# Kernel optimization log

Hardware: AMD Instinct MI355X
Metric: run time of the kernel (lower is better)

The kernel has to match this reference:

```python
import math
import jax, jax.numpy as jnp
import numpy as np

B, C, H, W = 8, 512, 32, 32
HEADS = 8


def _mix_rot(re, im, Wm, phi):
    # nn.Linear(dim, dim, bias=False) applied channelwise on [B,C,H,W]:
    # y = x @ Wm.T  ->  einsum over input channel c, output channel d
    re2 = jnp.einsum('bchw,dc->bdhw', re, Wm)
    im2 = jnp.einsum('bchw,dc->bdhw', im, Wm)
    c = jnp.cos(phi)[None, :, None, None]
    s = jnp.sin(phi)[None, :, None, None]
    # complex multiply (re2 + i*im2) * (cos phi + i*sin phi)
    return re2 * c - im2 * s, re2 * s + im2 * c


def setup_inputs() -> dict:
    key = jax.random.key(0)
    ks = jax.random.split(key, 6)
    scale = 1.0 / math.sqrt(C)
    return {
        'z_re': jax.random.normal(ks[0], (B, C, H, W), jnp.float32),
        'z_im': jax.random.normal(ks[1], (B, C, H, W), jnp.float32),
        'Wq': jax.random.normal(ks[2], (C, C), jnp.float32) * scale,
        'phi_q': jnp.zeros((C,), jnp.float32),
        'Wk': jax.random.normal(ks[3], (C, C), jnp.float32) * scale,
        'phi_k': jnp.zeros((C,), jnp.float32),
        'Wv': jax.random.normal(ks[4], (C, C), jnp.float32) * scale,
        'phi_v': jnp.zeros((C,), jnp.float32),
        'Wo': jax.random.normal(ks[5], (C, C), jnp.float32) * scale,
        'phi_o': jnp.zeros((C,), jnp.float32),
    }


def reference(z_re, z_im, Wq, phi_q, Wk, phi_k, Wv, phi_v, Wo, phi_o):
    b, c, h, w = z_re.shape
    T = h * w
    dh = c // HEADS

    def tok(a):  # [B,C,H,W] -> [B,T,C]
        return a.reshape(b, c, T).transpose(0, 2, 1)

    qre, qim = _mix_rot(z_re, z_im, Wq, phi_q)
    kre, kim = _mix_rot(z_re, z_im, Wk, phi_k)
    vre, vim = _mix_rot(z_re, z_im, Wv, phi_v)
    qre, qim = tok(qre), tok(qim)
    kre, kim = tok(kre), tok(kim)
    vre, vim = tok(vre), tok(vim)

    # real part of complex inner product: sums over FULL channel dim (no head split)
    scores = (jnp.einsum('btc,buc->btu', qre, kre)
              + jnp.einsum('btc,buc->btu', qim, kim)) / math.sqrt(dh)
    causal = jnp.triu(jnp.ones((T, T), bool), k=1)
    scores = jnp.where(causal[None], -jnp.inf, scores)
    attn = jax.nn.softmax(scores, axis=-1)

    out_re = jnp.einsum('btu,buc->btc', attn, vre)
    out_im = jnp.einsum('btu,buc->btc', attn, vim)

    def grid(a):  # [B,T,C] -> [B,C,H,W]
        return a.transpose(0, 2, 1).reshape(b, c, h, w)

    return _mix_rot(grid(out_re), grid(out_im), Wo, phi_o)
```

## Files before the change

kernel.cpp:

```cpp
#include <hip/hip_runtime.h>
#include <math.h>

#define NB 8
#define NC 512
#define NT 1024
#define BT (NB * NT)
#define SCALE 0.125f
#define NEG_BIG (-3.0e38f)

typedef __attribute__((ext_vector_type(8))) short short8v;
typedef __attribute__((ext_vector_type(8))) _Float16 half8v;
typedef __attribute__((ext_vector_type(4))) float float4v;
#define MFMA_BF16(A, B, C) __builtin_amdgcn_mfma_f32_16x16x32_bf16(A, B, C, 0, 0, 0)
#define MFMA_F16(A, B, C)  __builtin_amdgcn_mfma_f32_16x16x32_f16(A, B, C, 0, 0, 0)

__device__ __forceinline__ ushort f2bf(float f) {
    union { float f; unsigned int i; } v; v.f = f;
    unsigned int r = v.i + 0x7FFFu + ((v.i >> 16) & 1u);
    return (ushort)(r >> 16);
}

__device__ __forceinline__ ushort f2h(float f) {
    return __builtin_bit_cast(unsigned short, (_Float16)f);
}

__device__ __forceinline__ half8v scale8(short8v raw, float s) {
    half8v h = __builtin_bit_cast(half8v, raw);
    const _Float16 hs = (_Float16)s;
    half8v r;
    #pragma unroll
    for (int q = 0; q < 8; ++q) r[q] = h[q] * hs;
    return r;
}

#if defined(__has_builtin)
#if __has_builtin(__builtin_amdgcn_global_load_lds)
#define HAS_GLDS 1
#endif
#endif

#ifdef HAS_GLDS
__device__ __forceinline__ void glds16(const ushort* g, ushort* l) {
    __builtin_amdgcn_global_load_lds(
        (const __attribute__((address_space(1))) unsigned int*)g,
        (__attribute__((address_space(3))) unsigned int*)l, 16, 0, 0);
}
#endif

template<int ROWS>
__device__ __forceinline__ void stage64(const ushort* __restrict__ g, int rsShorts,
                                        ushort* tile, int w, int lane) {
    const int r8 = lane >> 3;
    const int ck = (lane & 7) ^ r8;
    const ushort* gl = g + (size_t)r8 * rsShorts + (ck << 3);
    constexpr int ni = ROWS / 32;
    #pragma unroll
    for (int s = 0; s < ni; ++s) {
        const int issue = w * ni + s;
#ifdef HAS_GLDS
        glds16(gl + (size_t)issue * 8 * rsShorts, tile + issue * 512);
#else
        const uint4 v = *(const uint4*)(gl + (size_t)issue * 8 * rsShorts);
        *(uint4*)(tile + issue * 512 + lane * 8) = v;
#endif
    }
}

__device__ __forceinline__ short8v frag(const ushort* tile, int rr, int q) {
    return *(const short8v*)(tile + rr * 64 + ((q ^ (rr & 7)) << 3));
}

__global__ __launch_bounds__(256) void prep_z_kernel(
    const float* __restrict__ zre, const float* __restrict__ zim,
    ushort* __restrict__ Z)
{
    const int t0 = blockIdx.x << 6, c0 = blockIdx.y << 6;
    const int bz = blockIdx.z, b = bz & 7, comp = bz >> 3;
    const float* src = (comp ? zim : zre) + (size_t)b * NC * NT;
    ushort* dst = Z + (size_t)(comp * NB + b) * NT * NC;
    const int tid = threadIdx.x;

    __shared__ ushort T[64][72];
    #pragma unroll
    for (int r = 0; r < 4; ++r) {
        const int cl = (tid >> 4) + r * 16;
        const int t4 = (tid & 15) << 2;
        const float4 v = *(const float4*)(src + (size_t)(c0 + cl) * NT + t0 + t4);
        T[t4 + 0][cl] = f2bf(v.x); T[t4 + 1][cl] = f2bf(v.y);
        T[t4 + 2][cl] = f2bf(v.z); T[t4 + 3][cl] = f2bf(v.w);
    }
    __syncthreads();
    const int tl = tid >> 2, cc = (tid & 3) << 4;
    ushort* op = dst + (size_t)(t0 + tl) * NC + c0 + cc;
    *(uint4*)op       = *(const uint4*)&T[tl][cc];
    *(uint4*)(op + 8) = *(const uint4*)&T[tl][cc + 8];
}

__global__ __launch_bounds__(256) void prep_w_kernel(
    const float* __restrict__ Wq, const float* __restrict__ Wk,
    const float* __restrict__ Wv, const float* __restrict__ Wo,
    ushort* __restrict__ Wbf)
{
    const int idx = blockIdx.x * 256 + threadIdx.x;
    const int e4 = idx << 2;
    const int m = e4 >> 18;
    const int off = e4 & ((1 << 18) - 1);
    const float* Ws[4] = {Wq, Wk, Wv, Wo};
    const float4 v = *(const float4*)(Ws[m] + off);
    ushort4 o;
    o.x = f2bf(v.x); o.y = f2bf(v.y); o.z = f2bf(v.z); o.w = f2bf(v.w);
    *(ushort4*)(Wbf + ((size_t)m << 18) + off) = o;
}

__global__ __launch_bounds__(256, 2) void proj_qk_kernel(
    const ushort* __restrict__ Z, const ushort* __restrict__ Wbf,
    const float* __restrict__ phiq, const float* __restrict__ phik,
    ushort* __restrict__ qre, ushort* __restrict__ qim,
    ushort* __restrict__ kre, ushort* __restrict__ kim)
{
    const int tid = threadIdx.x;
    const int m0 = blockIdx.x << 7;
    const int d0 = blockIdx.y << 6;
    const size_t NE = (size_t)BT * NC;

    __shared__ alignas(16) ushort SM[24576];
    ushort* Zr   = SM;
    ushort* Zi   = SM + 8192;
    ushort* Wq_s = SM + 16384;
    ushort* Wk_s = SM + 20480;
    uint*   R    = (uint*)SM;

    float4v accq[2][4][2] = {};
    float4v acck[2][4][2] = {};

    const int w = tid >> 6, lane = tid & 63;
    const int l15 = lane & 15, quad = lane >> 4;
    const int wm = (w & 1) << 6;
    const int wn = (w >> 1) << 5;

    for (int c0 = 0; c0 < NC; c0 += 64) {
        stage64<128>(Z + (size_t)m0 * NC + c0, NC, Zr, w, lane);
        stage64<128>(Z + NE + (size_t)m0 * NC + c0, NC, Zi, w, lane);
        stage64<64>(Wbf + (size_t)d0 * NC + c0, NC, Wq_s, w, lane);
        stage64<64>(Wbf + ((size_t)1 << 18) + (size_t)d0 * NC + c0, NC, Wk_s, w, lane);
        __syncthreads();
        #pragma unroll
        for (int kk = 0; kk < 2; ++kk) {
            const int q0 = kk * 4 + quad;
            short8v zf[2][4], wqf[2], wkf[2];
            #pragma unroll
            for (int i = 0; i < 4; ++i) {
                zf[0][i] = frag(Zr, wm + i * 16 + l15, q0);
                zf[1][i] = frag(Zi, wm + i * 16 + l15, q0);
            }
            #pragma unroll
            for (int j = 0; j < 2; ++j) {
                wqf[j] = frag(Wq_s, wn + j * 16 + l15, q0);
                wkf[j] = frag(Wk_s, wn + j * 16 + l15, q0);
            }
            #pragma unroll
            for (int c = 0; c < 2; ++c)
                #pragma unroll
                for (int i = 0; i < 4; ++i)
                    #pragma unroll
                    for (int j = 0; j < 2; ++j) {
                        accq[c][i][j] = MFMA_BF16(zf[c][i], wqf[j], accq[c][i][j]);
                        acck[c][i][j] = MFMA_BF16(zf[c][i], wkf[j], acck[c][i][j]);
                    }
        }
        __syncthreads();
    }

    float cq[2], sq[2], ck2[2], sk2[2];
    #pragma unroll
    for (int j = 0; j < 2; ++j) {
        const int d = d0 + wn + j * 16 + l15;
        const float pq = phiq[d], pk = phik[d];
        cq[j] = cosf(pq); sq[j] = sinf(pq);
        ck2[j] = cosf(pk); sk2[j] = sinf(pk);
    }
    const int g = tid >> 4, cl = tid & 15;

    #pragma unroll
    for (int j = 0; j < 2; ++j)
        #pragma unroll
        for (int i = 0; i < 4; ++i)
            #pragma unroll
            for (int r = 0; r < 4; ++r) {
                const int row = wm + i * 16 + quad * 4 + r;
                const int col = wn + j * 16 + l15;
                const float ar = accq[0][i][j][r], ai = accq[1][i][j][r];
                R[row * 76 + col] = (uint)f2bf(ar * cq[j] - ai * sq[j])
                                  | ((uint)f2bf(ar * sq[j] + ai * cq[j]) << 16);
            }
    __syncthreads();
    #pragma unroll
    for (int s = 0; s < 8; ++s) {
        const int row = g * 8 + s;
        const uint4 p = *(const uint4*)&R[row * 76 + cl * 4];
        uint2 re, im;
        re.x = (p.x & 0xFFFFu) | (p.y << 16);
        re.y = (p.z & 0xFFFFu) | (p.w << 16);
        im.x = (p.x >> 16) | (p.y & 0xFFFF0000u);
        im.y = (p.z >> 16) | (p.w & 0xFFFF0000u);
        const size_t off = (size_t)(m0 + row) * NC + d0 + cl * 4;
        *(uint2*)(qre + off) = re;
        *(uint2*)(qim + off) = im;
    }
    __syncthreads();

    #pragma unroll
    for (int j = 0; j < 2; ++j)
        #pragma unroll
        for (int i = 0; i < 4; ++i)
            #pragma unroll
            for (int r = 0; r < 4; ++r) {
                const int row = wm + i * 16 + quad * 4 + r;
                const int col = wn + j * 16 + l15;
                const float br = acck[0][i][j][r], bi = acck[1][i][j][r];
                R[row * 76 + col] = (uint)f2bf(br * ck2[j] - bi * sk2[j])
                                  | ((uint)f2bf(br * sk2[j] + bi * ck2[j]) << 16);
            }
    __syncthreads();
    #pragma unroll
    for (int s = 0; s < 8; ++s) {
        const int row = g * 8 + s;
        const uint4 p = *(const uint4*)&R[row * 76 + cl * 4];
        uint2 re, im;
        re.x = (p.x & 0xFFFFu) | (p.y << 16);
        re.y = (p.z & 0xFFFFu) | (p.w << 16);
        im.x = (p.x >> 16) | (p.y & 0xFFFF0000u);
        im.y = (p.z >> 16) | (p.w & 0xFFFF0000u);
        const size_t off = (size_t)(m0 + row) * NC + d0 + cl * 4;
        *(uint2*)(kre + off) = re;
        *(uint2*)(kim + off) = im;
    }
}

__global__ __launch_bounds__(256, 3) void proj_v_kernel(
    const ushort* __restrict__ Z, const ushort* __restrict__ Wbf,
    const float* __restrict__ phiv,
    ushort* __restrict__ vre, ushort* __restrict__ vim)
{
    const int tid = threadIdx.x;
    const int d0 = blockIdx.x << 7;
    const int bt0 = blockIdx.y << 6;
    const size_t NE = (size_t)BT * NC;

    __shared__ alignas(16) ushort SM[19456];
    ushort* Wv_s = SM;
    ushort* Zr   = SM + 8192;
    ushort* Zi   = SM + 12288;
    uint*   R    = (uint*)SM;

    float4v acc[2][4][2] = {};

    const int w = tid >> 6, lane = tid & 63;
    const int l15 = lane & 15, quad = lane >> 4;
    const int wm = (w & 1) << 6;
    const int wn = (w >> 1) << 5;

    for (int c0 = 0; c0 < NC; c0 += 64) {
        stage64<128>(Wbf + ((size_t)2 << 18) + (size_t)d0 * NC + c0, NC, Wv_s, w, lane);
        stage64<64>(Z + (size_t)bt0 * NC + c0, NC, Zr, w, lane);
        stage64<64>(Z + NE + (size_t)bt0 * NC + c0, NC, Zi, w, lane);
        __syncthreads();
        #pragma unroll
        for (int kk = 0; kk < 2; ++kk) {
            const int q0 = kk * 4 + quad;
            short8v wvf[4], zf[2][2];
            #pragma unroll
            for (int i = 0; i < 4; ++i)
                wvf[i] = frag(Wv_s, wm + i * 16 + l15, q0);
            #pragma unroll
            for (int j = 0; j < 2; ++j) {
                zf[0][j] = frag(Zr, wn + j * 16 + l15, q0);
                zf[1][j] = frag(Zi, wn + j * 16 + l15, q0);
            }
            #pragma unroll
            for (int c = 0; c < 2; ++c)
                #pragma unroll
                for (int i = 0; i < 4; ++i)
                    #pragma unroll
                    for (int j = 0; j < 2; ++j)
                        acc[c][i][j] = MFMA_BF16(wvf[i], zf[c][j], acc[c][i][j]);
        }
        __syncthreads();
    }

    const int d_own = d0 + wm + (l15 >> 2) * 16 + quad * 4 + (l15 & 3);
    const float ph_own = phiv[d_own];
    const float c_own = cosf(ph_own), s_own = sinf(ph_own);

    #pragma unroll
    for (int i = 0; i < 4; ++i)
        #pragma unroll
        for (int r = 0; r < 4; ++r) {
            const int src = (lane & 48) | (i * 4 + r);
            const float cs = __shfl(c_own, src, 64);
            const float sn = __shfl(s_own, src, 64);
            const int row = wm + i * 16 + quad * 4 + r;
            #pragma unroll
            for (int j = 0; j < 2; ++j) {
                const int col = wn + j * 16 + l15;
                const float vr = acc[0][i][j][r], vi = acc[1][i][j][r];
                R[row * 76 + col] = (uint)f2h(vr * cs - vi * sn)
                                  | ((uint)f2h(vr * sn + vi * cs) << 16);
            }
        }
    __syncthreads();
    const int g = tid >> 4, cl = tid & 15;
    const int b = bt0 >> 10, t0 = bt0 & 1023;
    #pragma unroll
    for (int s = 0; s < 8; ++s) {
        const int row = g * 8 + s;
        const uint4 p = *(const uint4*)&R[row * 76 + cl * 4];
        uint2 re, im;
        re.x = (p.x & 0xFFFFu) | (p.y << 16);
        re.y = (p.z & 0xFFFFu) | (p.w << 16);
        im.x = (p.x >> 16) | (p.y & 0xFFFF0000u);
        im.y = (p.z >> 16) | (p.w & 0xFFFF0000u);
        const size_t off = (size_t)b * NC * NT + (size_t)(d0 + row) * NT + t0 + cl * 4;
        *(uint2*)(vre + off) = re;
        *(uint2*)(vim + off) = im;
    }
}

__global__ __launch_bounds__(256, 3) void scores_kernel(
    const ushort* __restrict__ qre, const ushort* __restrict__ qim,
    const ushort* __restrict__ kre, const ushort* __restrict__ kim,
    ushort* __restrict__ Pp, float2* __restrict__ stats)
{
    const int u0b = blockIdx.x << 7;
    const int t0b = (gridDim.y - 1 - blockIdx.y) << 7;
    if (u0b > t0b) return;
    const int b = blockIdx.z;
    const int tid = threadIdx.x;
    const size_t qb = (size_t)b * NT * NC;

    __shared__ alignas(16) ushort SM[32768];
    ushort* Qr = SM;
    ushort* Qi = SM + 8192;
    ushort* Kr = SM + 16384;
    ushort* Ki = SM + 24576;
    ushort* Rs = SM;

    float4v acc[4][4] = {};

    const int w = tid >> 6, lane = tid & 63;
    const int l15 = lane & 15, quad = lane >> 4;
    const int wm = (w & 1) << 6;
    const int wn = (w >> 1) << 6;

    for (int c0 = 0; c0 < NC; c0 += 64) {
        stage64<128>(qre + qb + (size_t)t0b * NC + c0, NC, Qr, w, lane);
        stage64<128>(qim + qb + (size_t)t0b * NC + c0, NC, Qi, w, lane);
        stage64<128>(kre + qb + (size_t)u0b * NC + c0, NC, Kr, w, lane);
        stage64<128>(kim + qb + (size_t)u0b * NC + c0, NC, Ki, w, lane);
        __syncthreads();
        #pragma unroll
        for (int kk = 0; kk < 2; ++kk) {
            const int q0 = kk * 4 + quad;
            short8v qf[2][4], kf[2][4];
            #pragma unroll
            for (int i = 0; i < 4; ++i) {
                qf[0][i] = frag(Qr, wm + i * 16 + l15, q0);
                qf[1][i] = frag(Qi, wm + i * 16 + l15, q0);
                kf[0][i] = frag(Kr, wn + i * 16 + l15, q0);
                kf[1][i] = frag(Ki, wn + i * 16 + l15, q0);
            }
            #pragma unroll
            for (int i = 0; i < 4; ++i)
                #pragma unroll
                for (int j = 0; j < 4; ++j) {
                    acc[i][j] = MFMA_BF16(qf[0][i], kf[0][j], acc[i][j]);
                    acc[i][j] = MFMA_BF16(qf[1][i], kf[1][j], acc[i][j]);
                }
        }
        __syncthreads();
    }

    const int sub = (u0b + wn) >> 6;
    float2* st = stats + (size_t)(b * 16 + sub) * NT;
    #pragma unroll
    for (int i = 0; i < 4; ++i)
        #pragma unroll
        for (int r = 0; r < 4; ++r) {
            const int t = t0b + wm + i * 16 + quad * 4 + r;
            float v[4]; float m = NEG_BIG;
            #pragma unroll
            for (int j = 0; j < 4; ++j) {
                const int u = u0b + wn + j * 16 + l15;
                const float x = (u > t) ? NEG_BIG : acc[i][j][r] * SCALE;
                v[j] = x; m = fmaxf(m, x);
            }
            #pragma unroll
            for (int d = 1; d < 16; d <<= 1) m = fmaxf(m, __shfl_xor(m, d, 64));
            float l = 0.f;
            const int row = wm + i * 16 + quad * 4 + r;
            #pragma unroll
            for (int j = 0; j < 4; ++j) {
                const float e = __expf(v[j] - m);
                l += e;
                Rs[row * 140 + wn + j * 16 + l15] = f2h(e);
            }
            #pragma unroll
            for (int d = 1; d < 16; d <<= 1) l += __shfl_xor(l, d, 64);
            if (l15 == 0) st[t] = make_float2(m, l);
        }
    __syncthreads();
    ushort* Pb = Pp + (size_t)b * NT * NT;
    const int g = tid >> 5, cl = tid & 31;
    #pragma unroll
    for (int s = 0; s < 16; ++s) {
        const int row = g * 16 + s;
        const uint2 p = *(const uint2*)&Rs[row * 140 + cl * 4];
        *(uint2*)(Pb + (size_t)(t0b + row) * NT + u0b + cl * 4) = p;
    }
}

__global__ __launch_bounds__(256, 3) void pv_kernel(
    const ushort* __restrict__ Pp, const float2* __restrict__ stats,
    const ushort* __restrict__ vre, const ushort* __restrict__ vim,
    ushort* __restrict__ Ore, ushort* __restrict__ Oim)
{
    const int c0b = blockIdx.x << 6;
    const int t0b = (gridDim.y - 1 - blockIdx.y) << 7;
    const int b = blockIdx.z;
    const int tid = threadIdx.x;
    const ushort* P = Pp + ((size_t)b * NT + t0b) * NT;
    const size_t vb = (size_t)b * NC * NT;
    const int iters = (t0b + 128) >> 6;

    __shared__ alignas(16) ushort SM[20736];
    ushort* Ps = SM;
    ushort* Vr = SM + 8192;
    ushort* Vi = SM + 12288;
    float* sLds = (float*)(SM + 16384);
    uint*  R    = (uint*)SM;

    float4v acc[2][4][2] = {};

    const int w = tid >> 6, lane = tid & 63;
    const int l15 = lane & 15, quad = lane >> 4;
    const int wm = (w & 1) << 6;
    const int wn = (w >> 1) << 5;

    if (tid < 128) {
        const int t = t0b + tid;
        float mv[16], lv[16];
        #pragma unroll
        for (int s = 0; s < 16; ++s) {
            if (s < iters) {
                const float2 v = stats[(size_t)(b * 16 + s) * NT + t];
                mv[s] = v.x; lv[s] = v.y;
            } else { mv[s] = NEG_BIG; lv[s] = 0.f; }
        }
        float M = NEG_BIG;
        #pragma unroll
        for (int s = 0; s < 16; ++s) M = fmaxf(M, mv[s]);
        float L = 0.f; float ev[16];
        #pragma unroll
        for (int s = 0; s < 16; ++s) { ev[s] = __expf(mv[s] - M); L += ev[s] * lv[s]; }
        const float inv = 1.0f / L;
        #pragma unroll
        for (int s = 0; s < 16; ++s) sLds[tid * 17 + s] = ev[s] * inv;
    }

    for (int it = 0; it < iters; ++it) {
        const int u0 = it << 6;
        stage64<128>(P + u0, NT, Ps, w, lane);
        stage64<64>(vre + vb + (size_t)c0b * NT + u0, NT, Vr, w, lane);
        stage64<64>(vim + vb + (size_t)c0b * NT + u0, NT, Vi, w, lane);
        __syncthreads();
        #pragma unroll
        for (int kk = 0; kk < 2; ++kk) {
            const int q0 = kk * 4 + quad;
            half8v pf[4], vf[2][2];
            #pragma unroll
            for (int i = 0; i < 4; ++i) {
                const int row = wm + i * 16 + l15;
                pf[i] = scale8(frag(Ps, row, q0), sLds[row * 17 + it]);
            }
            #pragma unroll
            for (int j = 0; j < 2; ++j) {
                vf[0][j] = __builtin_bit_cast(half8v, frag(Vr, wn + j * 16 + l15, q0));
                vf[1][j] = __builtin_bit_cast(half8v, frag(Vi, wn + j * 16 + l15, q0));
            }
            #pragma unroll
            for (int c = 0; c < 2; ++c)
                #pragma unroll
                for (int i = 0; i < 4; ++i)
                    #pragma unroll
                    for (int j = 0; j < 2; ++j)
                        acc[c][i][j] = MFMA_F16(pf[i], vf[c][j], acc[c][i][j]);
        }
        __syncthreads();
    }

    #pragma unroll
    for (int i = 0; i < 4; ++i)
        #pragma unroll
        for (int j = 0; j < 2; ++j)
            #pragma unroll
            for (int r = 0; r < 4; ++r) {
                const int row = wm + i * 16 + quad * 4 + r;
                const int col = wn + j * 16 + l15;
                R[row * 76 + col] = (uint)f2bf(acc[0][i][j][r])
                                  | ((uint)f2bf(acc[1][i][j][r]) << 16);
            }
    __syncthreads();
    const int g = tid >> 4, cl = tid & 15;
    #pragma unroll
    for (int s = 0; s < 8; ++s) {
        const int row = g * 8 + s;
        const uint4 p = *(const uint4*)&R[row * 76 + cl * 4];
        uint2 re, im;
        re.x = (p.x & 0xFFFFu) | (p.y << 16);
        re.y = (p.z & 0xFFFFu) | (p.w << 16);
        im.x = (p.x >> 16) | (p.y & 0xFFFF0000u);
        im.y = (p.z >> 16) | (p.w & 0xFFFF0000u);
        const size_t off = ((size_t)b * NT + t0b + row) * NC + c0b + cl * 4;
        *(uint2*)(Ore + off) = re;
        *(uint2*)(Oim + off) = im;
    }
}

__global__ __launch_bounds__(256, 3) void proj_out_kernel(
    const ushort* __restrict__ Ore, const ushort* __restrict__ Oim,
    const ushort* __restrict__ Wbf, const float* __restrict__ phio,
    float* __restrict__ outRe, float* __restrict__ outIm)
{
    const int tid = threadIdx.x;
    const int d0 = blockIdx.x << 7;
    const int bt0 = blockIdx.y << 6;

    __shared__ alignas(16) ushort SM[19456];
    ushort* Wo_s = SM;
    ushort* Or_s = SM + 8192;
    ushort* Oi_s = SM + 12288;
    float*  Rf   = (float*)SM;

    float4v acc[2][4][2] = {};

    const int w = tid >> 6, lane = tid & 63;
    const int l15 = lane & 15, quad = lane >> 4;
    const int wm = (w & 1) << 6;
    const int wn = (w >> 1) << 5;

    for (int c0 = 0; c0 < NC; c0 += 64) {
        stage64<128>(Wbf + ((size_t)3 << 18) + (size_t)d0 * NC + c0, NC, Wo_s, w, lane);
        stage64<64>(Ore + (size_t)bt0 * NC + c0, NC, Or_s, w, lane);
        stage64<64>(Oim + (size_t)bt0 * NC + c0, NC, Oi_s, w, lane);
        __syncthreads();
        #pragma unroll
        for (int kk = 0; kk < 2; ++kk) {
            const int q0 = kk * 4 + quad;
            short8v wof[4], of[2][2];
            #pragma unroll
            for (int i = 0; i < 4; ++i)
                wof[i] = frag(Wo_s, wm + i * 16 + l15, q0);
            #pragma unroll
            for (int j = 0; j < 2; ++j) {
                of[0][j] = frag(Or_s, wn + j * 16 + l15, q0);
                of[1][j] = frag(Oi_s, wn + j * 16 + l15, q0);
            }
            #pragma unroll
            for (int c = 0; c < 2; ++c)
                #pragma unroll
                for (int i = 0; i < 4; ++i)
                    #pragma unroll
                    for (int j = 0; j < 2; ++j)
                        acc[c][i][j] = MFMA_BF16(wof[i], of[c][j], acc[c][i][j]);
        }
        __syncthreads();
    }

    const int d_own = d0 + wm + (l15 >> 2) * 16 + quad * 4 + (l15 & 3);
    const float ph_own = phio[d_own];
    const float c_own = cosf(ph_own), s_own = sinf(ph_own);
    const int g = tid >> 4, cl = tid & 15;
    const int b = bt0 >> 10, t0 = bt0 & 1023;

    #pragma unroll
    for (int i = 0; i < 4; ++i)
        #pragma unroll
        for (int r = 0; r < 4; ++r) {
            const int src = (lane & 48) | (i * 4 + r);
            const float cs = __shfl(c_own, src, 64);
            const float sn = __shfl(s_own, src, 64);
            const int row = wm + i * 16 + quad * 4 + r;
            #pragma unroll
            for (int j = 0; j < 2; ++j) {
                const int col = wn + j * 16 + l15;
                Rf[row * 76 + col] = acc[0][i][j][r] * cs - acc[1][i][j][r] * sn;
            }
        }
    __syncthreads();
    #pragma unroll
    for (int s = 0; s < 8; ++s) {
        const int row = g * 8 + s;
        const float4 p = *(const float4*)&Rf[row * 76 + cl * 4];
        *(float4*)(outRe + (size_t)b * NC * NT + (size_t)(d0 + row) * NT + t0 + cl * 4) = p;
    }
    __syncthreads();

    #pragma unroll
    for (int i = 0; i < 4; ++i)
        #pragma unroll
        for (int r = 0; r < 4; ++r) {
            const int src = (lane & 48) | (i * 4 + r);
            const float cs = __shfl(c_own, src, 64);
            const float sn = __shfl(s_own, src, 64);
            const int row = wm + i * 16 + quad * 4 + r;
            #pragma unroll
            for (int j = 0; j < 2; ++j) {
                const int col = wn + j * 16 + l15;
                Rf[row * 76 + col] = acc[0][i][j][r] * sn + acc[1][i][j][r] * cs;
            }
        }
    __syncthreads();
    #pragma unroll
    for (int s = 0; s < 8; ++s) {
        const int row = g * 8 + s;
        const float4 p = *(const float4*)&Rf[row * 76 + cl * 4];
        *(float4*)(outIm + (size_t)b * NC * NT + (size_t)(d0 + row) * NT + t0 + cl * 4) = p;
    }
}

extern "C" void kernel_launch(void* const* d_in, const int* in_sizes, int n_in,
                              void* d_out, int out_size, void* d_ws, size_t ws_size,
                              hipStream_t stream) {
    (void)in_sizes; (void)n_in; (void)out_size; (void)ws_size;
    const float* z_re  = (const float*)d_in[0];
    const float* z_im  = (const float*)d_in[1];
    const float* Wq    = (const float*)d_in[2];
    const float* phi_q = (const float*)d_in[3];
    const float* Wk    = (const float*)d_in[4];
    const float* phi_k = (const float*)d_in[5];
    const float* Wv    = (const float*)d_in[6];
    const float* phi_v = (const float*)d_in[7];
    const float* Wo    = (const float*)d_in[8];
    const float* phi_o = (const float*)d_in[9];

    const size_t NE = (size_t)BT * NC;
    ushort* ws  = (ushort*)d_ws;
    ushort* qre = ws + 0 * NE; ushort* qim = ws + 1 * NE;
    ushort* kre = ws + 2 * NE; ushort* kim = ws + 3 * NE;
    ushort* vre = ws + 4 * NE; ushort* vim = ws + 5 * NE;
    ushort* Wbf = ws + 6 * NE;
    ushort* Z  = (ushort*)d_out;
    ushort* Pp = (ushort*)d_out + 2 * NE;
    float2* stats = (float2*)d_out;

    const dim3 blk(256);
    hipLaunchKernelGGL(prep_z_kernel, dim3(NT / 64, NC / 64, NB * 2), blk, 0, stream, z_re, z_im, Z);
    hipLaunchKernelGGL(prep_w_kernel, dim3(1024), blk, 0, stream, Wq, Wk, Wv, Wo, Wbf);
    hipLaunchKernelGGL(proj_qk_kernel, dim3(BT / 128, NC / 64), blk, 0, stream,
                       Z, Wbf, phi_q, phi_k, qre, qim, kre, kim);
    hipLaunchKernelGGL(proj_v_kernel, dim3(NC / 128, BT / 64), blk, 0, stream,
                       Z, Wbf, phi_v, vre, vim);
    hipLaunchKernelGGL(scores_kernel, dim3(NT / 128, NT / 128, NB), blk, 0, stream,
                       qre, qim, kre, kim, Pp, stats);
    hipLaunchKernelGGL(pv_kernel, dim3(NC / 64, NT / 128, NB), blk, 0, stream,
                       Pp, stats, vre, vim, qre, qim);
    hipLaunchKernelGGL(proj_out_kernel, dim3(NC / 128, BT / 64), blk, 0, stream,
                       qre, qim, Wbf, phi_o, (float*)d_out, (float*)d_out + NE);
}
```

Before: 210.8 us.

## Swizzle block indices across XCDs and split scores staging into re/im passes

Adds an XCD-aware block-index remapping to the projection, scores, PV and output kernels, so blocks that share input tiles are placed on the same XCD and can reuse its L2. The scores kernel now stages the real and imaginary Q/K tiles in two passes over a smaller shared-memory buffer instead of all four at once. This cuts LDS use per block, which may allow more resident blocks per CU, at the cost of extra barriers per channel chunk. The swizzle assumes each grid's block count is divisible by 8.

```diff
diff --git a/kernel.cpp b/kernel.cpp
--- a/kernel.cpp
+++ b/kernel.cpp
@@ -68,6 +68,10 @@
 
 __device__ __forceinline__ short8v frag(const ushort* tile, int rr, int q) {
     return *(const short8v*)(tile + rr * 64 + ((q ^ (rr & 7)) << 3));
+}
+
+__device__ __forceinline__ int xcd_swz(int flat, int cpx) {
+    return (flat & 7) * cpx + (flat >> 3);
 }
 
 __global__ __launch_bounds__(256) void prep_z_kernel(
@@ -119,8 +123,9 @@
     ushort* __restrict__ kre, ushort* __restrict__ kim)
 {
     const int tid = threadIdx.x;
-    const int m0 = blockIdx.x << 7;
-    const int d0 = blockIdx.y << 6;
+    const int swz = xcd_swz(blockIdx.x + 64 * blockIdx.y, 64);
+    const int m0 = (swz & 63) << 7;
+    const int d0 = (swz >> 6) << 6;
     const size_t NE = (size_t)BT * NC;
 
     __shared__ alignas(16) ushort SM[24576];
@@ -243,8 +248,9 @@
     ushort* __restrict__ vre, ushort* __restrict__ vim)
 {
     const int tid = threadIdx.x;
-    const int d0 = blockIdx.x << 7;
-    const int bt0 = blockIdx.y << 6;
+    const int swz = xcd_swz(blockIdx.x + 4 * blockIdx.y, 64);
+    const int d0 = (swz & 3) << 7;
+    const int bt0 = (swz >> 2) << 6;
     const size_t NE = (size_t)BT * NC;
 
     __shared__ alignas(16) ushort SM[19456];
@@ -331,18 +337,17 @@
     const ushort* __restrict__ kre, const ushort* __restrict__ kim,
     ushort* __restrict__ Pp, float2* __restrict__ stats)
 {
-    const int u0b = blockIdx.x << 7;
-    const int t0b = (gridDim.y - 1 - blockIdx.y) << 7;
+    const int swz = xcd_swz(blockIdx.x + 8 * (blockIdx.y + 8 * blockIdx.z), 64);
+    const int u0b = (swz & 7) << 7;
+    const int t0b = (7 - ((swz >> 3) & 7)) << 7;
     if (u0b > t0b) return;
-    const int b = blockIdx.z;
+    const int b = swz >> 6;
     const int tid = threadIdx.x;
     const size_t qb = (size_t)b * NT * NC;
 
-    __shared__ alignas(16) ushort SM[32768];
-    ushort* Qr = SM;
-    ushort* Qi = SM + 8192;
-    ushort* Kr = SM + 16384;
-    ushort* Ki = SM + 24576;
+    __shared__ alignas(16) ushort SM[17920];
+    ushort* Qs = SM;
+    ushort* Ks = SM + 8192;
     ushort* Rs = SM;
 
     float4v acc[4][4] = {};
@@ -353,29 +358,42 @@
     const int wn = (w >> 1) << 6;
 
     for (int c0 = 0; c0 < NC; c0 += 64) {
-        stage64<128>(qre + qb + (size_t)t0b * NC + c0, NC, Qr, w, lane);
-        stage64<128>(qim + qb + (size_t)t0b * NC + c0, NC, Qi, w, lane);
-        stage64<128>(kre + qb + (size_t)u0b * NC + c0, NC, Kr, w, lane);
-        stage64<128>(kim + qb + (size_t)u0b * NC + c0, NC, Ki, w, lane);
+        stage64<128>(qre + qb + (size_t)t0b * NC + c0, NC, Qs, w, lane);
+        stage64<128>(kre + qb + (size_t)u0b * NC + c0, NC, Ks, w, lane);
         __syncthreads();
         #pragma unroll
         for (int kk = 0; kk < 2; ++kk) {
             const int q0 = kk * 4 + quad;
-            short8v qf[2][4], kf[2][4];
+            short8v qf[4], kf[4];
             #pragma unroll
             for (int i = 0; i < 4; ++i) {
-                qf[0][i] = frag(Qr, wm + i * 16 + l15, q0);
-                qf[1][i] = frag(Qi, wm + i * 16 + l15, q0);
-                kf[0][i] = frag(Kr, wn + i * 16 + l15, q0);
-                kf[1][i] = frag(Ki, wn + i * 16 + l15, q0);
+                qf[i] = frag(Qs, wm + i * 16 + l15, q0);
+                kf[i] = frag(Ks, wn + i * 16 + l15, q0);
             }
             #pragma unroll
             for (int i = 0; i < 4; ++i)
                 #pragma unroll
-                for (int j = 0; j < 4; ++j) {
-                    acc[i][j] = MFMA_BF16(qf[0][i], kf[0][j], acc[i][j]);
-                    acc[i][j] = MFMA_BF16(qf[1][i], kf[1][j], acc[i][j]);
-                }
+                for (int j = 0; j < 4; ++j)
+                    acc[i][j] = MFMA_BF16(qf[i], kf[j], acc[i][j]);
+        }
+        __syncthreads();
+        stage64<128>(qim + qb + (size_t)t0b * NC + c0, NC, Qs, w, lane);
+        stage64<128>(kim + qb + (size_t)u0b * NC + c0, NC, Ks, w, lane);
+        __syncthreads();
+        #pragma unroll
+        for (int kk = 0; kk < 2; ++kk) {
+            const int q0 = kk * 4 + quad;
+            short8v qf[4], kf[4];
+            #pragma unroll
+            for (int i = 0; i < 4; ++i) {
+                qf[i] = frag(Qs, wm + i * 16 + l15, q0);
+                kf[i] = frag(Ks, wn + i * 16 + l15, q0);
+            }
+            #pragma unroll
+            for (int i = 0; i < 4; ++i)
+                #pragma unroll
+                for (int j = 0; j < 4; ++j)
+                    acc[i][j] = MFMA_BF16(qf[i], kf[j], acc[i][j]);
         }
         __syncthreads();
     }
@@ -424,9 +442,10 @@
     const ushort* __restrict__ vre, const ushort* __restrict__ vim,
     ushort* __restrict__ Ore, ushort* __restrict__ Oim)
 {
-    const int c0b = blockIdx.x << 6;
-    const int t0b = (gridDim.y - 1 - blockIdx.y) << 7;
-    const int b = blockIdx.z;
+    const int swz = xcd_swz(blockIdx.x + 8 * (blockIdx.y + 8 * blockIdx.z), 64);
+    const int c0b = (swz & 7) << 6;
+    const int t0b = (7 - ((swz >> 3) & 7)) << 7;
+    const int b = swz >> 6;
     const int tid = threadIdx.x;
     const ushort* P = Pp + ((size_t)b * NT + t0b) * NT;
     const size_t vb = (size_t)b * NC * NT;
@@ -532,8 +551,9 @@
     float* __restrict__ outRe, float* __restrict__ outIm)
 {
     const int tid = threadIdx.x;
-    const int d0 = blockIdx.x << 7;
-    const int bt0 = blockIdx.y << 6;
+    const int swz = xcd_swz(blockIdx.x + 4 * blockIdx.y, 64);
+    const int d0 = (swz & 3) << 7;
+    const int bt0 = (swz >> 2) << 6;
 
     __shared__ alignas(16) ushort SM[19456];
     ushort* Wo_s = SM;
```

New measurement: 206.0 us. -2.3%, faster.
